# Kernel optimization log

Hardware: AMD Instinct MI355X
Metric: run time of the kernel (lower is better)

## Reference

```python
import jax, jax.numpy as jnp
import numpy as np

B, L, C = 8, 1024, 1152
H = 16
D = C // H
FF = int(C * 4.0)
EPS = 1e-6


def _layernorm(x):
    # LayerNorm without affine params, eps=1e-6
    mu = jnp.mean(x, axis=-1, keepdims=True)
    var = jnp.mean(jnp.square(x - mu), axis=-1, keepdims=True)
    return (x - mu) * jax.lax.rsqrt(var + EPS)


def _modulate(x, shift, scale):
    return x * (1.0 + scale) + shift


def setup_inputs() -> dict:
    key = jax.random.key(0)
    ks = jax.random.split(key, 12)
    s = 0.02
    return {
        "x": jax.random.normal(ks[0], (B, L, C), jnp.float32),
        "c": jax.random.normal(ks[1], (B, 1, C), jnp.float32),
        "W_qkv": jax.random.normal(ks[2], (C, 3 * C), jnp.float32) * s,
        "b_qkv": jnp.zeros((3 * C,), jnp.float32),
        "W_proj": jax.random.normal(ks[3], (C, C), jnp.float32) * s,
        "b_proj": jnp.zeros((C,), jnp.float32),
        "W_fc1": jax.random.normal(ks[4], (C, FF), jnp.float32) * s,
        "b_fc1": jnp.zeros((FF,), jnp.float32),
        "W_fc2": jax.random.normal(ks[5], (FF, C), jnp.float32) * s,
        "b_fc2": jnp.zeros((C,), jnp.float32),
        "W_ada": jax.random.normal(ks[6], (C, 6 * C), jnp.float32) * s,
        "b_ada": jnp.zeros((6 * C,), jnp.float32),
    }


def _attention(h, W_qkv, b_qkv, W_proj, b_proj):
    b, l, c = h.shape
    qkv = h @ W_qkv + b_qkv                      # (B,L,3C)
    qkv = qkv.reshape(b, l, 3, H, D)
    q, k, v = qkv[:, :, 0], qkv[:, :, 1], qkv[:, :, 2]  # (B,L,H,D)
    scale = D ** (-0.5)
    scores = jnp.einsum("blhd,bmhd->bhlm", q * scale, k)  # (B,H,L,L)
    attn = jax.nn.softmax(scores, axis=-1)
    o = jnp.einsum("bhlm,bmhd->blhd", attn, v).reshape(b, l, c)
    return o @ W_proj + b_proj


def reference(x, c, W_qkv, b_qkv, W_proj, b_proj, W_fc1, b_fc1, W_fc2, b_fc2, W_ada, b_ada):
    ada = jax.nn.silu(c) @ W_ada + b_ada         # (B,1,6C)
    (shift_msa, scale_msa, gate_msa,
     shift_mlp, scale_mlp, gate_mlp) = jnp.split(ada, 6, axis=-1)

    h = _modulate(_layernorm(x), shift_msa, scale_msa)
    x = x + gate_msa * _attention(h, W_qkv, b_qkv, W_proj, b_proj)

    h = _modulate(_layernorm(x), shift_mlp, scale_mlp)
    mlp = jax.nn.gelu(h @ W_fc1 + b_fc1, approximate=True) @ W_fc2 + b_fc2
    x = x + gate_mlp * mlp
    return x
```

## Files before the change

kernel.cpp:

```cpp
#include <hip/hip_runtime.h>
#include <stdint.h>

#define DEV static __device__ __forceinline__

typedef __attribute__((ext_vector_type(8))) __bf16 bf16x8;
typedef __attribute__((ext_vector_type(4))) float f32x4;
typedef unsigned short u16;
typedef unsigned int u32;

DEV u16 f2b(float f) {
  u32 u = __float_as_uint(f);
  u32 r = (u + 0x7FFFu + ((u >> 16) & 1u)) >> 16;
  return (u16)r;
}

DEV void gload16(const u16* g, u16* l) {
  __builtin_amdgcn_global_load_lds(
      (const __attribute__((address_space(1))) u32*)g,
      (__attribute__((address_space(3))) u32*)l, 16, 0, 0);
}

__global__ __launch_bounds__(256) void wt_bf16(const float* __restrict__ W,
                                               u16* __restrict__ Wt, int K, int N) {
  __shared__ float t[32][33];
  int n0 = blockIdx.x * 32, k0 = blockIdx.y * 32;
  int tx = threadIdx.x & 31, ty = threadIdx.x >> 5;
#pragma unroll
  for (int i = 0; i < 32; i += 8)
    t[ty + i][tx] = W[(long)(k0 + ty + i) * N + n0 + tx];
  __syncthreads();
#pragma unroll
  for (int i = 0; i < 32; i += 8)
    Wt[(long)(n0 + ty + i) * K + k0 + tx] = f2b(t[tx][ty + i]);
}

__global__ __launch_bounds__(512) void ada_gemm(const float* __restrict__ c,
                                                const float* __restrict__ W,
                                                const float* __restrict__ bias,
                                                float* __restrict__ ada) {
  __shared__ float sc[8 * 1152];
  int t = threadIdx.x;
  for (int i = t; i < 8 * 1152; i += 512) {
    float v = c[i];
    sc[i] = v / (1.f + __expf(-v));
  }
  __syncthreads();
  int n = blockIdx.x * 64 + (t & 63), b = t >> 6;
  const float* wp = W + n;
  const float* scp = sc + b * 1152;
  float acc = 0.f;
#pragma unroll 8
  for (int k = 0; k < 1152; ++k) acc = fmaf(scp[k], wp[(long)k * 6912], acc);
  ada[b * 6912 + n] = acc + bias[n];
}

__global__ __launch_bounds__(256) void ln_mod(const float* __restrict__ X,
                                              const float* __restrict__ ada,
                                              int so, int co, u16* __restrict__ out) {
  int r = blockIdx.x, b = r >> 10, t = threadIdx.x;
  const float4* xr = (const float4*)(X + (long)r * 1152);
  float4 v0 = xr[t];
  float4 v1 = make_float4(0.f, 0.f, 0.f, 0.f);
  bool two = t < 32;
  if (two) v1 = xr[256 + t];
  float s = v0.x + v0.y + v0.z + v0.w + v1.x + v1.y + v1.z + v1.w;
  float q = v0.x * v0.x + v0.y * v0.y + v0.z * v0.z + v0.w * v0.w +
            v1.x * v1.x + v1.y * v1.y + v1.z * v1.z + v1.w * v1.w;
#pragma unroll
  for (int m = 32; m > 0; m >>= 1) { s += __shfl_xor(s, m); q += __shfl_xor(q, m); }
  __shared__ float ss[4], sq[4];
  if ((t & 63) == 0) { ss[t >> 6] = s; sq[t >> 6] = q; }
  __syncthreads();
  s = ss[0] + ss[1] + ss[2] + ss[3];
  q = sq[0] + sq[1] + sq[2] + sq[3];
  const float inv = 1.f / 1152.f;
  float mu = s * inv;
  float var = q * inv - mu * mu;
  float rs = rsqrtf(var + 1e-6f);
  const float4* sh = (const float4*)(ada + b * 6912 + so);
  const float4* sc = (const float4*)(ada + b * 6912 + co);
  u16* orow = out + (long)r * 1152;
  {
    float4 hv = sh[t], cv = sc[t];
    union { u16 u[4]; uint2 d; } p;
    p.u[0] = f2b((v0.x - mu) * rs * (1.f + cv.x) + hv.x);
    p.u[1] = f2b((v0.y - mu) * rs * (1.f + cv.y) + hv.y);
    p.u[2] = f2b((v0.z - mu) * rs * (1.f + cv.z) + hv.z);
    p.u[3] = f2b((v0.w - mu) * rs * (1.f + cv.w) + hv.w);
    ((uint2*)orow)[t] = p.d;
  }
  if (two) {
    float4 hv = sh[256 + t], cv = sc[256 + t];
    union { u16 u[4]; uint2 d; } p;
    p.u[0] = f2b((v1.x - mu) * rs * (1.f + cv.x) + hv.x);
    p.u[1] = f2b((v1.y - mu) * rs * (1.f + cv.y) + hv.y);
    p.u[2] = f2b((v1.z - mu) * rs * (1.f + cv.z) + hv.z);
    p.u[3] = f2b((v1.w - mu) * rs * (1.f + cv.w) + hv.w);
    ((uint2*)orow)[256 + t] = p.d;
  }
}

__global__ __launch_bounds__(256) void transpose_v(const u16* __restrict__ V,
                                                   u16* __restrict__ Vt) {
  __shared__ u16 t[32][33];
  long zofs = (long)blockIdx.z * 98304;
  int d0 = blockIdx.x * 32, l0 = blockIdx.y * 32;
  int tx = threadIdx.x & 31, ty = threadIdx.x >> 5;
#pragma unroll
  for (int i = 0; i < 32; i += 8)
    t[ty + i][tx] = V[zofs + (long)(l0 + ty + i) * 96 + d0 + tx];
  __syncthreads();
#pragma unroll
  for (int i = 0; i < 32; i += 8)
    Vt[zofs + (long)(d0 + ty + i) * 1024 + l0 + tx] = t[tx][ty + i];
}

__global__ __launch_bounds__(256, 2) void flash_attn(
    const u16* __restrict__ Q, const u16* __restrict__ K,
    const u16* __restrict__ Vt, u16* __restrict__ Oa) {
  __shared__ __align__(16) u16 Plds[4][4096];
  const int lane = threadIdx.x & 63, w = threadIdx.x >> 6;
  const int lr = lane & 15, lg = lane >> 4;
  const int bh = blockIdx.y;
  const int q0 = blockIdx.x * 128 + w * 32;
  const u16* Qp = Q + (long)bh * 98304;
  const u16* Kp = K + (long)bh * 98304;
  const u16* Vp = Vt + (long)bh * 98304;
  char* pl = (char*)&Plds[w][0];

  bf16x8 qf[2][3];
#pragma unroll
  for (int i = 0; i < 2; ++i)
#pragma unroll
    for (int kk = 0; kk < 3; ++kk)
      qf[i][kk] = *(const bf16x8*)(Qp + (long)(q0 + i * 16 + lr) * 96 + kk * 32 + lg * 8);

  f32x4 o[2][5] = {};
  float mrow[2][4], lrow[2][4];
#pragma unroll
  for (int i = 0; i < 2; ++i)
#pragma unroll
    for (int r = 0; r < 4; ++r) { mrow[i][r] = -3e38f; lrow[i][r] = 0.f; }

  for (int kt = 0; kt < 8; ++kt) {
    const int kv0 = kt * 128;
    f32x4 s[2][8] = {};
    __builtin_amdgcn_s_setprio(1);
#pragma unroll
    for (int j = 0; j < 8; ++j) {
      const u16* kp = Kp + (long)(kv0 + j * 16 + lr) * 96 + lg * 8;
      bf16x8 k0 = *(const bf16x8*)kp;
      bf16x8 k1 = *(const bf16x8*)(kp + 32);
      bf16x8 k2 = *(const bf16x8*)(kp + 64);
#pragma unroll
      for (int i = 0; i < 2; ++i) {
        s[i][j] = __builtin_amdgcn_mfma_f32_16x16x32_bf16(qf[i][0], k0, s[i][j], 0, 0, 0);
        s[i][j] = __builtin_amdgcn_mfma_f32_16x16x32_bf16(qf[i][1], k1, s[i][j], 0, 0, 0);
        s[i][j] = __builtin_amdgcn_mfma_f32_16x16x32_bf16(qf[i][2], k2, s[i][j], 0, 0, 0);
      }
    }
    __builtin_amdgcn_s_setprio(0);
    float mx[2][4];
#pragma unroll
    for (int i = 0; i < 2; ++i)
#pragma unroll
      for (int r = 0; r < 4; ++r) {
        float m0 = s[i][0][r];
#pragma unroll
        for (int j = 1; j < 8; ++j) m0 = fmaxf(m0, s[i][j][r]);
        mx[i][r] = m0;
      }
#pragma unroll
    for (int mk = 1; mk < 16; mk <<= 1)
#pragma unroll
      for (int i = 0; i < 2; ++i)
#pragma unroll
        for (int r = 0; r < 4; ++r) mx[i][r] = fmaxf(mx[i][r], __shfl_xor(mx[i][r], mk));
#pragma unroll
    for (int i = 0; i < 2; ++i)
#pragma unroll
      for (int r = 0; r < 4; ++r) {
        float nm = fmaxf(mrow[i][r], mx[i][r]);
        float sc = __expf(mrow[i][r] - nm);
        mrow[i][r] = nm;
        lrow[i][r] *= sc;
#pragma unroll
        for (int n = 0; n < 5; ++n) o[i][n][r] *= sc;
      }
    float ps[2][4] = {};
#pragma unroll
    for (int i = 0; i < 2; ++i)
#pragma unroll
      for (int j = 0; j < 8; ++j)
#pragma unroll
        for (int r = 0; r < 4; ++r) {
          float p = __expf(s[i][j][r] - mrow[i][r]);
          ps[i][r] += p;
          const int row = i * 16 + lg * 4 + r;
          const int byte = (row * 256 + (j * 16 + lr) * 2) ^ ((row & 7) << 4);
          *(u16*)(pl + byte) = f2b(p);
        }
#pragma unroll
    for (int mk = 1; mk < 16; mk <<= 1)
#pragma unroll
      for (int i = 0; i < 2; ++i)
#pragma unroll
        for (int r = 0; r < 4; ++r) ps[i][r] += __shfl_xor(ps[i][r], mk);
#pragma unroll
    for (int i = 0; i < 2; ++i)
#pragma unroll
      for (int r = 0; r < 4; ++r) lrow[i][r] += ps[i][r];
    bf16x8 pa[2][4];
#pragma unroll
    for (int i = 0; i < 2; ++i)
#pragma unroll
      for (int ks = 0; ks < 4; ++ks) {
        const int byte = ((i * 16 + lr) * 256 + (ks * 32 + lg * 8) * 2) ^ ((lr & 7) << 4);
        pa[i][ks] = *(const bf16x8*)(pl + byte);
      }
    __builtin_amdgcn_s_setprio(1);
#pragma unroll
    for (int n = 0; n < 5; ++n) {
#pragma unroll
      for (int ks = 0; ks < 4; ++ks) {
        bf16x8 vf = *(const bf16x8*)(Vp + (long)(n * 16 + lr) * 1024 + kv0 + ks * 32 + lg * 8);
#pragma unroll
        for (int i = 0; i < 2; ++i)
          o[i][n] = __builtin_amdgcn_mfma_f32_16x16x32_bf16(pa[i][ks], vf, o[i][n], 0, 0, 0);
      }
    }
    __builtin_amdgcn_s_setprio(0);
  }
  const int b = bh >> 4, h = bh & 15;
#pragma unroll
  for (int i = 0; i < 2; ++i)
#pragma unroll
    for (int r = 0; r < 4; ++r) {
      const int l = q0 + i * 16 + lg * 4 + r;
      const float rinv = 1.f / lrow[i][r];
      u16* orow = Oa + ((long)b * 1024 + l) * 1152 + h * 72;
#pragma unroll
      for (int n = 0; n < 5; ++n) {
        const int col = n * 16 + lr;
        if (col < 72) orow[col] = f2b(o[i][n][r] * rinv);
      }
    }
}

template <int TM, int TN, int MODE>
__global__ __launch_bounds__(256) void gemm_bt(
    const u16* __restrict__ A, const u16* __restrict__ Bt, int Kd, int ldc,
    const float* __restrict__ bias, void* __restrict__ outp,
    const float* __restrict__ res, const float* __restrict__ ada, int gofs,
    u16* __restrict__ qb, u16* __restrict__ kb, u16* __restrict__ vb) {
  constexpr int BM = TM * 32, BN = TN * 32;
  __shared__ __align__(16) u16 lA[BM * 32];
  __shared__ __align__(16) u16 lB[BN * 32];
  const int tid = threadIdx.x, lane = tid & 63, w = tid >> 6;
  const int wr = w >> 1, wc = w & 1, lr = lane & 15, lg = lane >> 4;
  const u16* Ab = A + (long)blockIdx.x * BM * Kd;
  const u16* Bb = Bt + (long)blockIdx.y * BN * Kd;
  const int srow = lane >> 2, scol = (lane & 3) * 8;
  const u16* ga0 = Ab + (long)srow * Kd + scol;
  const u16* gb0 = Bb + (long)srow * Kd + scol;

  f32x4 acc[TM][TN] = {};
  const int nk = Kd >> 5;
  for (int kt = 0; kt < nk; ++kt) {
    for (int ch = w; ch < BM / 16; ch += 4)
      gload16(ga0 + (long)(ch * 16) * Kd + kt * 32, &lA[ch * 512]);
    for (int ch = w; ch < BN / 16; ch += 4)
      gload16(gb0 + (long)(ch * 16) * Kd + kt * 32, &lB[ch * 512]);
    __syncthreads();
    bf16x8 af[TM], bfr[TN];
#pragma unroll
    for (int i = 0; i < TM; ++i)
      af[i] = *(const bf16x8*)&lA[(wr * TM * 16 + i * 16 + lr) * 32 + lg * 8];
#pragma unroll
    for (int j = 0; j < TN; ++j)
      bfr[j] = *(const bf16x8*)&lB[(wc * TN * 16 + j * 16 + lr) * 32 + lg * 8];
#pragma unroll
    for (int i = 0; i < TM; ++i)
#pragma unroll
      for (int j = 0; j < TN; ++j)
        acc[i][j] = __builtin_amdgcn_mfma_f32_16x16x32_bf16(af[i], bfr[j], acc[i][j], 0, 0, 0);
    __syncthreads();
  }

#pragma unroll
  for (int i = 0; i < TM; ++i) {
#pragma unroll
    for (int j = 0; j < TN; ++j) {
#pragma unroll
      for (int r = 0; r < 4; ++r) {
        const int row = blockIdx.x * BM + wr * TM * 16 + i * 16 + lg * 4 + r;
        const int col = blockIdx.y * BN + wc * TN * 16 + j * 16 + lr;
        float val = acc[i][j][r];
        if (MODE == 1) {
          val += bias[col];
          int sel = col / 1152, cc = col - sel * 1152;
          int hh = cc / 72, dd = cc - hh * 72;
          int bb = row >> 10, ll = row & 1023;
          long idx = ((long)(bb * 16 + hh) * 1024 + ll) * 96 + dd;
          if (sel == 0) qb[idx] = f2b(val * 0.11785113019775793f);
          else if (sel == 1) kb[idx] = f2b(val);
          else vb[idx] = f2b(val);
        } else if (MODE == 3 || MODE == 5) {
          val += bias[col];
          float* o = (float*)outp;
          long idx = (long)row * 1152 + col;
          o[idx] = res[idx] + ada[(row >> 10) * 6912 + gofs + col] * val;
        } else if (MODE == 4) {
          val += bias[col];
          float t2 = 0.7978845608028654f * (val + 0.044715f * val * val * val);
          t2 = fminf(fmaxf(t2, -15.f), 15.f);
          float e2 = __expf(2.f * t2);
          float th = 1.f - 2.f / (e2 + 1.f);
          ((u16*)outp)[(long)row * ldc + col] = f2b(0.5f * val * (1.f + th));
        }
      }
    }
  }
}

extern "C" void kernel_launch(void* const* d_in, const int* in_sizes, int n_in,
                              void* d_out, int out_size, void* d_ws, size_t ws_size,
                              hipStream_t stream) {
  const float* x    = (const float*)d_in[0];
  const float* c    = (const float*)d_in[1];
  const float* Wqkv = (const float*)d_in[2];
  const float* bqkv = (const float*)d_in[3];
  const float* Wprj = (const float*)d_in[4];
  const float* bprj = (const float*)d_in[5];
  const float* Wfc1 = (const float*)d_in[6];
  const float* bfc1 = (const float*)d_in[7];
  const float* Wfc2 = (const float*)d_in[8];
  const float* bfc2 = (const float*)d_in[9];
  const float* Wada = (const float*)d_in[10];
  const float* bada = (const float*)d_in[11];

  char* ws = (char*)d_ws;
  size_t o = 0;
  auto alloc = [&](size_t bytes) -> char* {
    char* p = ws + o;
    o += (bytes + 255) & ~(size_t)255;
    return p;
  };
  u16* wqkvT = (u16*)alloc(3456ull * 1152 * 2);
  u16* wprjT = (u16*)alloc(1152ull * 1152 * 2);
  u16* wfc1T = (u16*)alloc(4608ull * 1152 * 2);
  u16* wfc2T = (u16*)alloc(1152ull * 4608 * 2);
  float* adab = (float*)alloc(8ull * 6912 * 4);
  u16* hbuf = (u16*)alloc(8192ull * 1152 * 2);
  u16* Qb   = (u16*)alloc(25165824);
  u16* Kb   = (u16*)alloc(25165824);
  u16* Vt   = (u16*)alloc(25165824);
  u16* attn = (u16*)alloc(8192ull * 1152 * 2);
  float* x2 = (float*)alloc(8192ull * 1152 * 4);
  u16* Vb = (u16*)x2;
  u16* hmid = Qb;

  wt_bf16<<<dim3(108, 36), 256, 0, stream>>>(Wqkv, wqkvT, 1152, 3456);
  wt_bf16<<<dim3(36, 36), 256, 0, stream>>>(Wprj, wprjT, 1152, 1152);
  wt_bf16<<<dim3(144, 36), 256, 0, stream>>>(Wfc1, wfc1T, 1152, 4608);
  wt_bf16<<<dim3(36, 144), 256, 0, stream>>>(Wfc2, wfc2T, 4608, 1152);
  ada_gemm<<<108, 512, 0, stream>>>(c, Wada, bada, adab);
  hipMemsetAsync(Qb, 0, 2ull * 25165824, stream);
  hipMemsetAsync(Vb, 0, 25165824, stream);
  ln_mod<<<8192, 256, 0, stream>>>(x, adab, 0, 1152, hbuf);
  gemm_bt<4, 4, 1><<<dim3(64, 27), 256, 0, stream>>>(
      hbuf, wqkvT, 1152, 0, bqkv, nullptr, nullptr, nullptr, 0, Qb, Kb, Vb);
  transpose_v<<<dim3(3, 32, 128), 256, 0, stream>>>(Vb, Vt);
  flash_attn<<<dim3(8, 128), 256, 0, stream>>>(Qb, Kb, Vt, attn);
  gemm_bt<2, 4, 3><<<dim3(128, 9), 256, 0, stream>>>(
      attn, wprjT, 1152, 1152, bprj, x2, x, adab, 2304, nullptr, nullptr, nullptr);
  ln_mod<<<8192, 256, 0, stream>>>(x2, adab, 3456, 4608, hbuf);
  gemm_bt<4, 4, 4><<<dim3(64, 36), 256, 0, stream>>>(
      hbuf, wfc1T, 1152, 4608, bfc1, hmid, nullptr, nullptr, 0, nullptr, nullptr, nullptr);
  gemm_bt<4, 2, 5><<<dim3(64, 18), 256, 0, stream>>>(
      hmid, wfc2T, 4608, 1152, bfc2, d_out, x2, adab, 5760, nullptr, nullptr, nullptr);
}
```

Measured before the change: 955.6 us.

## Double-buffer GEMM LDS staging and split-K the fc2 GEMM with atomics

The bf16 GEMM kernel now keeps two LDS buffers. The next K-tile is loaded asynchronously while the current one feeds the MFMAs, so there is one barrier per iteration instead of two, which aims to hide global-load latency. The fc2 GEMM moves to a larger 4x4 tile and splits K in two across blockIdx.z, with each split atomically adding its gated partial sum into the output. A new out_init kernel first writes residual plus gate times bias into the output. This trades extra atomic traffic, an extra elementwise pass and doubled LDS use per block for better load overlap and more parallelism on the long-K GEMM.

```diff
diff --git a/kernel.cpp b/kernel.cpp
--- a/kernel.cpp
+++ b/kernel.cpp
@@ -100,6 +100,22 @@
   }
 }
 
+__global__ __launch_bounds__(256) void out_init(const float* __restrict__ res,
+                                                const float* __restrict__ ada,
+                                                const float* __restrict__ bias,
+                                                float* __restrict__ out) {
+  int r = blockIdx.x, b = r >> 10, t = threadIdx.x;
+  const float4* rr = (const float4*)(res + (long)r * 1152);
+  const float4* bb = (const float4*)bias;
+  const float4* gg = (const float4*)(ada + b * 6912 + 5760);
+  float4* oo = (float4*)(out + (long)r * 1152);
+  for (int i = t; i < 288; i += 256) {
+    float4 rv = rr[i], bv = bb[i], gv = gg[i];
+    oo[i] = make_float4(rv.x + gv.x * bv.x, rv.y + gv.y * bv.y,
+                        rv.z + gv.z * bv.z, rv.w + gv.w * bv.w);
+  }
+}
+
 __global__ __launch_bounds__(256) void transpose_v(const u16* __restrict__ V,
                                                    u16* __restrict__ Vt) {
   __shared__ u16 t[32][33];
@@ -250,35 +266,42 @@
 template <int TM, int TN, int MODE>
 __global__ __launch_bounds__(256) void gemm_bt(
     const u16* __restrict__ A, const u16* __restrict__ Bt, int Kd, int ldc,
-    const float* __restrict__ bias, void* __restrict__ outp,
+    int ksplit, const float* __restrict__ bias, void* __restrict__ outp,
     const float* __restrict__ res, const float* __restrict__ ada, int gofs,
     u16* __restrict__ qb, u16* __restrict__ kb, u16* __restrict__ vb) {
   constexpr int BM = TM * 32, BN = TN * 32;
-  __shared__ __align__(16) u16 lA[BM * 32];
-  __shared__ __align__(16) u16 lB[BN * 32];
+  __shared__ __align__(16) u16 lA[2][BM * 32];
+  __shared__ __align__(16) u16 lB[2][BN * 32];
   const int tid = threadIdx.x, lane = tid & 63, w = tid >> 6;
   const int wr = w >> 1, wc = w & 1, lr = lane & 15, lg = lane >> 4;
-  const u16* Ab = A + (long)blockIdx.x * BM * Kd;
-  const u16* Bb = Bt + (long)blockIdx.y * BN * Kd;
+  const int nk = (Kd / ksplit) >> 5;
+  const long k0 = (long)blockIdx.z * (Kd / ksplit);
+  const u16* Ab = A + (long)blockIdx.x * BM * Kd + k0;
+  const u16* Bb = Bt + (long)blockIdx.y * BN * Kd + k0;
   const int srow = lane >> 2, scol = (lane & 3) * 8;
   const u16* ga0 = Ab + (long)srow * Kd + scol;
   const u16* gb0 = Bb + (long)srow * Kd + scol;
 
+  auto stage = [&](int buf, int kt) {
+    for (int ch = w; ch < BM / 16; ch += 4)
+      gload16(ga0 + (long)(ch * 16) * Kd + kt * 32, &lA[buf][ch * 512]);
+    for (int ch = w; ch < BN / 16; ch += 4)
+      gload16(gb0 + (long)(ch * 16) * Kd + kt * 32, &lB[buf][ch * 512]);
+  };
+
   f32x4 acc[TM][TN] = {};
-  const int nk = Kd >> 5;
+  stage(0, 0);
+  __syncthreads();
   for (int kt = 0; kt < nk; ++kt) {
-    for (int ch = w; ch < BM / 16; ch += 4)
-      gload16(ga0 + (long)(ch * 16) * Kd + kt * 32, &lA[ch * 512]);
-    for (int ch = w; ch < BN / 16; ch += 4)
-      gload16(gb0 + (long)(ch * 16) * Kd + kt * 32, &lB[ch * 512]);
-    __syncthreads();
+    const int cur = kt & 1;
+    if (kt + 1 < nk) stage(cur ^ 1, kt + 1);
     bf16x8 af[TM], bfr[TN];
 #pragma unroll
     for (int i = 0; i < TM; ++i)
-      af[i] = *(const bf16x8*)&lA[(wr * TM * 16 + i * 16 + lr) * 32 + lg * 8];
+      af[i] = *(const bf16x8*)&lA[cur][(wr * TM * 16 + i * 16 + lr) * 32 + lg * 8];
 #pragma unroll
     for (int j = 0; j < TN; ++j)
-      bfr[j] = *(const bf16x8*)&lB[(wc * TN * 16 + j * 16 + lr) * 32 + lg * 8];
+      bfr[j] = *(const bf16x8*)&lB[cur][(wc * TN * 16 + j * 16 + lr) * 32 + lg * 8];
 #pragma unroll
     for (int i = 0; i < TM; ++i)
 #pragma unroll
@@ -305,7 +328,7 @@
           if (sel == 0) qb[idx] = f2b(val * 0.11785113019775793f);
           else if (sel == 1) kb[idx] = f2b(val);
           else vb[idx] = f2b(val);
-        } else if (MODE == 3 || MODE == 5) {
+        } else if (MODE == 3) {
           val += bias[col];
           float* o = (float*)outp;
           long idx = (long)row * 1152 + col;
@@ -317,6 +340,10 @@
           float e2 = __expf(2.f * t2);
           float th = 1.f - 2.f / (e2 + 1.f);
           ((u16*)outp)[(long)row * ldc + col] = f2b(0.5f * val * (1.f + th));
+        } else if (MODE == 6) {
+          float* o = (float*)outp;
+          long idx = (long)row * 1152 + col;
+          atomicAdd(&o[idx], ada[(row >> 10) * 6912 + gofs + col] * val);
         }
       }
     }
@@ -369,14 +396,16 @@
   hipMemsetAsync(Vb, 0, 25165824, stream);
   ln_mod<<<8192, 256, 0, stream>>>(x, adab, 0, 1152, hbuf);
   gemm_bt<4, 4, 1><<<dim3(64, 27), 256, 0, stream>>>(
-      hbuf, wqkvT, 1152, 0, bqkv, nullptr, nullptr, nullptr, 0, Qb, Kb, Vb);
+      hbuf, wqkvT, 1152, 0, 1, bqkv, nullptr, nullptr, nullptr, 0, Qb, Kb, Vb);
   transpose_v<<<dim3(3, 32, 128), 256, 0, stream>>>(Vb, Vt);
   flash_attn<<<dim3(8, 128), 256, 0, stream>>>(Qb, Kb, Vt, attn);
   gemm_bt<2, 4, 3><<<dim3(128, 9), 256, 0, stream>>>(
-      attn, wprjT, 1152, 1152, bprj, x2, x, adab, 2304, nullptr, nullptr, nullptr);
+      attn, wprjT, 1152, 1152, 1, bprj, x2, x, adab, 2304, nullptr, nullptr, nullptr);
   ln_mod<<<8192, 256, 0, stream>>>(x2, adab, 3456, 4608, hbuf);
   gemm_bt<4, 4, 4><<<dim3(64, 36), 256, 0, stream>>>(
-      hbuf, wfc1T, 1152, 4608, bfc1, hmid, nullptr, nullptr, 0, nullptr, nullptr, nullptr);
-  gemm_bt<4, 2, 5><<<dim3(64, 18), 256, 0, stream>>>(
-      hmid, wfc2T, 4608, 1152, bfc2, d_out, x2, adab, 5760, nullptr, nullptr, nullptr);
-}
+      hbuf, wfc1T, 1152, 4608, 1, bfc1, hmid, nullptr, nullptr, 0, nullptr, nullptr, nullptr);
+  out_init<<<8192, 256, 0, stream>>>(x2, adab, bfc2, (float*)d_out);
+  gemm_bt<4, 4, 6><<<dim3(64, 9, 2), 256, 0, stream>>>(
+      hmid, wfc2T, 4608, 1152, 2, nullptr, d_out, nullptr, adab, 5760,
+      nullptr, nullptr, nullptr);
+}
```

Result: no change. 945.4 us (-1.1%).
